# Kernel tuning notes

Measured on AMD Instinct MI355X. Metric: run time of the kernel, lower is better.

The kernel has to match this reference:

```python
import jax, jax.numpy as jnp
import numpy as np


def setup_inputs() -> dict:
    key = jax.random.key(0)
    k1, k2, k3 = jax.random.split(key, 3)
    vol_shape = (4, 1, 128, 192, 192)   # [B, C, D, H, W]
    dsc_shape = (4, 1, 8, 12, 12)       # PatchGAN-style discriminator logits
    return {
        "dsc_fake": jax.random.normal(k1, dsc_shape, dtype=jnp.float32),
        "predicts": jax.random.normal(k2, vol_shape, dtype=jnp.float32),
        "y_data": jax.random.normal(k3, vol_shape, dtype=jnp.float32),
        "zeros": jnp.zeros(dsc_shape, dtype=jnp.float32),
    }


def reference(dsc_fake, predicts, y_data, zeros):
    # BCE with logits (stable form), target = zeros
    bce = jnp.mean(
        jnp.maximum(dsc_fake, 0.0) - dsc_fake * zeros
        + jnp.log1p(jnp.exp(-jnp.abs(dsc_fake)))
    )
    # L1 loss between target volume and prediction
    g_loss_l1 = jnp.mean(jnp.abs(y_data - predicts))
    # Finite-difference gradient MSE along D, H, W (axes 2,3,4).
    # Original detaches to numpy, so this term carries no gradient.
    yd = jax.lax.stop_gradient(y_data)
    pr = jax.lax.stop_gradient(predicts)
    g_loss_gd = jnp.float32(0.0)
    for ax in (2, 3, 4):
        gy = jnp.abs(jnp.gradient(yd, axis=ax))   # central diff interior, one-sided edges
        gp = jnp.abs(jnp.gradient(pr, axis=ax))
        g_loss_gd = g_loss_gd + jnp.mean((gy - gp) ** 2)
    return bce + 100.0 * g_loss_l1 + 100.0 * g_loss_gd
```

## Files before the change

kernel.cpp:

```cpp
#include <hip/hip_runtime.h>
#include <math.h>

namespace {
constexpr int BATCH = 4;
constexpr int DDIM  = 128;
constexpr int HDIM  = 192;
constexpr int WDIM  = 192;
constexpr long long NTOT = (long long)BATCH * DDIM * HDIM * WDIM;
constexpr int GW   = WDIM / 4;
constexpr int HS4  = GW;
constexpr int DS4  = GW * HDIM;
constexpr int NDSC = 4 * 1 * 8 * 12 * 12;
constexpr int BLOCK = 256;
constexpr int DC    = 8;
constexpr int NCH   = DDIM / DC;
constexpr int NCOL  = BATCH * HDIM * GW;
constexpr int NTHREADS = NCOL * NCH;
constexpr int GRID  = NTHREADS / BLOCK;
}

__device__ __forceinline__ float4 ld4(const float* __restrict__ p, long long g) {
    return *(const float4*)(p + 4LL * g);
}

__global__ __launch_bounds__(BLOCK) void vol_kernel(const float* __restrict__ p,
                                                    const float* __restrict__ y,
                                                    float* __restrict__ part) {
    const int t   = blockIdx.x * BLOCK + threadIdx.x;
    const int gw  = t % GW;
    int rest      = t / GW;
    const int h   = rest % HDIM; rest /= HDIM;
    const int b   = rest % BATCH;
    const int d0  = (rest / BATCH) * DC;

    const int   hmo = (h > 0)        ? HS4 : 0;
    const int   hpo = (h < HDIM - 1) ? HS4 : 0;
    const float sh  = (h == 0 || h == HDIM - 1) ? 1.f : 0.5f;
    const int   wlo = (gw > 0)       ? -1 : 0;
    const int   wro = (gw < GW - 1)  ? 4 : 3;
    const float swx = (gw == 0)      ? 1.f : 0.5f;
    const float sww = (gw == GW - 1) ? 1.f : 0.5f;

    long long g = (((long long)b * DDIM + d0) * HDIM + h) * GW + gw;

    const long long gm = g - ((d0 > 0) ? DS4 : 0);
    float4 ym = ld4(y, gm), pm = ld4(p, gm);
    float4 yc = ld4(y, g),  pc = ld4(p, g);
    long long gn = g + DS4;
    float4 yn = ld4(y, gn), pn = ld4(p, gn);
    float4 yhm = ld4(y, g - hmo), yhp = ld4(y, g + hpo);
    float4 phm = ld4(p, g - hmo), php = ld4(p, g + hpo);
    float ywl = y[4LL * g + wlo], ywr = y[4LL * g + wro];
    float pwl = p[4LL * g + wlo], pwr = p[4LL * g + wro];

    float l1 = 0.f, gd = 0.f;

    #pragma unroll
    for (int i = 0; i < DC; ++i) {
        const int d = d0 + i;

        float4 ynn, pnn, yhm2, yhp2, phm2, php2;
        float ywl2, ywr2, pwl2, pwr2;
        long long gnn = gn;
        if (i < DC - 1) {
            gnn = gn + ((d + 2 < DDIM) ? DS4 : 0);
            ynn  = ld4(y, gnn);      pnn  = ld4(p, gnn);
            yhm2 = ld4(y, gn - hmo); yhp2 = ld4(y, gn + hpo);
            phm2 = ld4(p, gn - hmo); php2 = ld4(p, gn + hpo);
            ywl2 = y[4LL * gn + wlo]; ywr2 = y[4LL * gn + wro];
            pwl2 = p[4LL * gn + wlo]; pwr2 = p[4LL * gn + wro];
        }

        const float sd = (d == 0 || d == DDIM - 1) ? 1.f : 0.5f;

        l1 += fabsf(yc.x - pc.x) + fabsf(yc.y - pc.y)
            + fabsf(yc.z - pc.z) + fabsf(yc.w - pc.w);

        float t0, gy, gp;
        gy = (yc.y - ywl) * swx;  gp = (pc.y - pwl) * swx;
        t0 = fabsf(gy) - fabsf(gp); gd += t0 * t0;
        gy = (yc.z - yc.x) * 0.5f; gp = (pc.z - pc.x) * 0.5f;
        t0 = fabsf(gy) - fabsf(gp); gd += t0 * t0;
        gy = (yc.w - yc.y) * 0.5f; gp = (pc.w - pc.y) * 0.5f;
        t0 = fabsf(gy) - fabsf(gp); gd += t0 * t0;
        gy = (ywr - yc.z) * sww;  gp = (pwr - pc.z) * sww;
        t0 = fabsf(gy) - fabsf(gp); gd += t0 * t0;

        t0 = fabsf((yhp.x - yhm.x) * sh) - fabsf((php.x - phm.x) * sh); gd += t0 * t0;
        t0 = fabsf((yhp.y - yhm.y) * sh) - fabsf((php.y - phm.y) * sh); gd += t0 * t0;
        t0 = fabsf((yhp.z - yhm.z) * sh) - fabsf((php.z - phm.z) * sh); gd += t0 * t0;
        t0 = fabsf((yhp.w - yhm.w) * sh) - fabsf((php.w - phm.w) * sh); gd += t0 * t0;

        t0 = fabsf((yn.x - ym.x) * sd) - fabsf((pn.x - pm.x) * sd); gd += t0 * t0;
        t0 = fabsf((yn.y - ym.y) * sd) - fabsf((pn.y - pm.y) * sd); gd += t0 * t0;
        t0 = fabsf((yn.z - ym.z) * sd) - fabsf((pn.z - pm.z) * sd); gd += t0 * t0;
        t0 = fabsf((yn.w - ym.w) * sd) - fabsf((pn.w - pm.w) * sd); gd += t0 * t0;

        if (i < DC - 1) {
            ym = yc; yc = yn; yn = ynn;
            pm = pc; pc = pn; pn = pnn;
            yhm = yhm2; yhp = yhp2; phm = phm2; php = php2;
            ywl = ywl2; ywr = ywr2; pwl = pwl2; pwr = pwr2;
            g = gn; gn = gnn;
        }
    }

    __shared__ float lds1[4], lds2[4];
    #pragma unroll
    for (int off = 32; off > 0; off >>= 1) {
        l1 += __shfl_down(l1, off, 64);
        gd += __shfl_down(gd, off, 64);
    }
    if ((threadIdx.x & 63) == 0) {
        lds1[threadIdx.x >> 6] = l1;
        lds2[threadIdx.x >> 6] = gd;
    }
    __syncthreads();
    if (threadIdx.x == 0) {
        part[2 * blockIdx.x]     = lds1[0] + lds1[1] + lds1[2] + lds1[3];
        part[2 * blockIdx.x + 1] = lds2[0] + lds2[1] + lds2[2] + lds2[3];
    }
}

__global__ __launch_bounds__(BLOCK) void finalize_kernel(const float* __restrict__ dsc,
                                                         const float* __restrict__ part,
                                                         float* __restrict__ out) {
    float l1 = 0.f, gd = 0.f, s = 0.f;
    for (int i = threadIdx.x; i < GRID; i += BLOCK) {
        l1 += part[2 * i];
        gd += part[2 * i + 1];
    }
    for (int i = threadIdx.x; i < NDSC; i += BLOCK) {
        const float x = dsc[i];
        s += fmaxf(x, 0.f) + log1pf(expf(-fabsf(x)));
    }
    __shared__ float a[4], c[4], e[4];
    #pragma unroll
    for (int off = 32; off > 0; off >>= 1) {
        l1 += __shfl_down(l1, off, 64);
        gd += __shfl_down(gd, off, 64);
        s  += __shfl_down(s,  off, 64);
    }
    if ((threadIdx.x & 63) == 0) {
        const int w = threadIdx.x >> 6;
        a[w] = l1; c[w] = gd; e[w] = s;
    }
    __syncthreads();
    if (threadIdx.x == 0) {
        const float bce = (e[0] + e[1] + e[2] + e[3]) / (float)NDSC;
        const float l1m = (a[0] + a[1] + a[2] + a[3]) / (float)NTOT;
        const float gdm = (c[0] + c[1] + c[2] + c[3]) / (float)NTOT;
        out[0] = bce + 100.f * (l1m + gdm);
    }
}

extern "C" void kernel_launch(void* const* d_in, const int* in_sizes, int n_in,
                              void* d_out, int out_size, void* d_ws, size_t ws_size,
                              hipStream_t stream) {
    const float* dsc_fake = (const float*)d_in[0];
    const float* predicts = (const float*)d_in[1];
    const float* y_data   = (const float*)d_in[2];
    float* part = (float*)d_ws;
    float* out  = (float*)d_out;

    vol_kernel<<<GRID, BLOCK, 0, stream>>>(predicts, y_data, part);
    finalize_kernel<<<1, BLOCK, 0, stream>>>(dsc_fake, part, out);
}
```

Measured before the change: 193.4 us.

## Stage HxW slabs in LDS via async global_load_lds with triple-buffered D sweep

The volume kernel now gives each block a 12-row H tile with halo across 16 D planes. Each plane of y and p is staged into LDS with async global-to-LDS loads in a three-deep ring, and H/W neighbours are read from shared memory instead of re-read from global. This cuts the redundant global traffic of the old per-thread stencil, which loaded H neighbours and W edge scalars separately, and overlaps plane prefetch with compute using explicit waitcnt and barriers. The cost is large LDS use per block, a smaller grid of 512 blocks of 192 threads, and fragile hand-written vmcnt accounting.

Result: no change. 190.2 us (-1.6%).

```diff
diff --git a/kernel.cpp b/kernel.cpp
--- a/kernel.cpp
+++ b/kernel.cpp
@@ -7,134 +7,198 @@
 constexpr int HDIM  = 192;
 constexpr int WDIM  = 192;
 constexpr long long NTOT = (long long)BATCH * DDIM * HDIM * WDIM;
-constexpr int GW   = WDIM / 4;
-constexpr int HS4  = GW;
-constexpr int DS4  = GW * HDIM;
-constexpr int NDSC = 4 * 1 * 8 * 12 * 12;
-constexpr int BLOCK = 256;
-constexpr int DC    = 8;
-constexpr int NCH   = DDIM / DC;
-constexpr int NCOL  = BATCH * HDIM * GW;
-constexpr int NTHREADS = NCOL * NCH;
-constexpr int GRID  = NTHREADS / BLOCK;
-}
-
-__device__ __forceinline__ float4 ld4(const float* __restrict__ p, long long g) {
-    return *(const float4*)(p + 4LL * g);
-}
-
-__global__ __launch_bounds__(BLOCK) void vol_kernel(const float* __restrict__ p,
-                                                    const float* __restrict__ y,
-                                                    float* __restrict__ part) {
-    const int t   = blockIdx.x * BLOCK + threadIdx.x;
-    const int gw  = t % GW;
-    int rest      = t / GW;
-    const int h   = rest % HDIM; rest /= HDIM;
-    const int b   = rest % BATCH;
-    const int d0  = (rest / BATCH) * DC;
-
-    const int   hmo = (h > 0)        ? HS4 : 0;
-    const int   hpo = (h < HDIM - 1) ? HS4 : 0;
-    const float sh  = (h == 0 || h == HDIM - 1) ? 1.f : 0.5f;
-    const int   wlo = (gw > 0)       ? -1 : 0;
-    const int   wro = (gw < GW - 1)  ? 4 : 3;
-    const float swx = (gw == 0)      ? 1.f : 0.5f;
-    const float sww = (gw == GW - 1) ? 1.f : 0.5f;
-
-    long long g = (((long long)b * DDIM + d0) * HDIM + h) * GW + gw;
-
-    const long long gm = g - ((d0 > 0) ? DS4 : 0);
-    float4 ym = ld4(y, gm), pm = ld4(p, gm);
-    float4 yc = ld4(y, g),  pc = ld4(p, g);
-    long long gn = g + DS4;
-    float4 yn = ld4(y, gn), pn = ld4(p, gn);
-    float4 yhm = ld4(y, g - hmo), yhp = ld4(y, g + hpo);
-    float4 phm = ld4(p, g - hmo), php = ld4(p, g + hpo);
-    float ywl = y[4LL * g + wlo], ywr = y[4LL * g + wro];
-    float pwl = p[4LL * g + wlo], pwr = p[4LL * g + wro];
+constexpr int NDSC  = 4 * 1 * 8 * 12 * 12;
+
+constexpr int HT     = 12;
+constexpr int DT     = 16;
+constexpr int ROWS   = HT + 2;
+constexpr int SLABF  = ROWS * WDIM;
+constexpr int SLAB2  = 2 * SLABF;
+constexpr int BLOCKV = 192;
+constexpr int GRIDV  = BATCH * (DDIM / DT) * (HDIM / HT);
+constexpr int UPW    = 7;
+constexpr int PLSTR  = HDIM * WDIM;
+constexpr int BLOCKF = 256;
+}
+
+#define GTERM(dy, dp, s2) { float t0_ = fabsf(dy) - fabsf(dp); gd = fmaf(t0_ * t0_, (s2), gd); }
+
+#define STAGE(buf, plane)                                                      \
+    {                                                                          \
+        const int poff_ = (plane) * PLSTR;                                     \
+        _Pragma("unroll")                                                      \
+        for (int k = 0; k < UPW; ++k) {                                        \
+            __builtin_amdgcn_global_load_lds(                                  \
+                (const __attribute__((address_space(1))) void*)(sr[k] + poff_),\
+                (__attribute__((address_space(3))) void*)(                     \
+                    &slab[buf][0] + (wv * UPW + k) * 256),                     \
+                16, 0, 0);                                                     \
+        }                                                                      \
+    }
+
+__global__ __launch_bounds__(BLOCKV) void vol_kernel(const float* __restrict__ p,
+                                                     const float* __restrict__ y,
+                                                     float* __restrict__ part) {
+    __shared__ float slab[3][SLAB2];
+    __shared__ float red[2][3];
+
+    const int tid  = threadIdx.x;
+    const int wv   = tid >> 6;
+    const int lane = tid & 63;
+    const int r    = tid >> 4;
+    const int i16  = tid & 15;
+    const int w0   = i16 * 12;
+
+    const int blk = blockIdx.x;
+    const int ht = blk & 15;
+    const int dc = (blk >> 4) & 7;
+    const int b  = blk >> 7;
+    const int h0 = ht * HT;
+    const int d0 = dc * DT;
+    const int h  = h0 + r;
+
+    const float* sr[UPW];
+    #pragma unroll
+    for (int k = 0; k < UPW; ++k) {
+        const int u   = wv * UPW + k;
+        const int fi  = u * 256 + lane * 4;
+        const int ts  = fi >= SLABF;
+        const int fj  = ts ? fi - SLABF : fi;
+        const int row = fj / WDIM;
+        const int col = fj - row * WDIM;
+        int hrow = h0 - 1 + row;
+        hrow = hrow < 0 ? 0 : (hrow > HDIM - 1 ? HDIM - 1 : hrow);
+        sr[k] = (ts ? p : y) + (b * DDIM * HDIM + hrow) * WDIM + col;
+    }
+
+    float4 ym[2][3], yc[2][3];
+    {
+        const int pmz = d0 ? d0 - 1 : 0;
+        const int om = ((b * DDIM + pmz) * HDIM + h) * WDIM + w0;
+        const int oc = ((b * DDIM + d0 ) * HDIM + h) * WDIM + w0;
+        #pragma unroll
+        for (int g = 0; g < 3; ++g) {
+            ym[0][g] = *(const float4*)(y + om + 4 * g);
+            ym[1][g] = *(const float4*)(p + om + 4 * g);
+            yc[0][g] = *(const float4*)(y + oc + 4 * g);
+            yc[1][g] = *(const float4*)(p + oc + 4 * g);
+        }
+    }
+    STAGE(0, d0);
+    STAGE(1, d0 + 1);
+    STAGE(2, d0 + 2);
 
     float l1 = 0.f, gd = 0.f;
-
-    #pragma unroll
-    for (int i = 0; i < DC; ++i) {
-        const int d = d0 + i;
-
-        float4 ynn, pnn, yhm2, yhp2, phm2, php2;
-        float ywl2, ywr2, pwl2, pwr2;
-        long long gnn = gn;
-        if (i < DC - 1) {
-            gnn = gn + ((d + 2 < DDIM) ? DS4 : 0);
-            ynn  = ld4(y, gnn);      pnn  = ld4(p, gnn);
-            yhm2 = ld4(y, gn - hmo); yhp2 = ld4(y, gn + hpo);
-            phm2 = ld4(p, gn - hmo); php2 = ld4(p, gn + hpo);
-            ywl2 = y[4LL * gn + wlo]; ywr2 = y[4LL * gn + wro];
-            pwl2 = p[4LL * gn + wlo]; pwr2 = p[4LL * gn + wro];
-        }
-
-        const float sd = (d == 0 || d == DDIM - 1) ? 1.f : 0.5f;
-
-        l1 += fabsf(yc.x - pc.x) + fabsf(yc.y - pc.y)
-            + fabsf(yc.z - pc.z) + fabsf(yc.w - pc.w);
-
-        float t0, gy, gp;
-        gy = (yc.y - ywl) * swx;  gp = (pc.y - pwl) * swx;
-        t0 = fabsf(gy) - fabsf(gp); gd += t0 * t0;
-        gy = (yc.z - yc.x) * 0.5f; gp = (pc.z - pc.x) * 0.5f;
-        t0 = fabsf(gy) - fabsf(gp); gd += t0 * t0;
-        gy = (yc.w - yc.y) * 0.5f; gp = (pc.w - pc.y) * 0.5f;
-        t0 = fabsf(gy) - fabsf(gp); gd += t0 * t0;
-        gy = (ywr - yc.z) * sww;  gp = (pwr - pc.z) * sww;
-        t0 = fabsf(gy) - fabsf(gp); gd += t0 * t0;
-
-        t0 = fabsf((yhp.x - yhm.x) * sh) - fabsf((php.x - phm.x) * sh); gd += t0 * t0;
-        t0 = fabsf((yhp.y - yhm.y) * sh) - fabsf((php.y - phm.y) * sh); gd += t0 * t0;
-        t0 = fabsf((yhp.z - yhm.z) * sh) - fabsf((php.z - phm.z) * sh); gd += t0 * t0;
-        t0 = fabsf((yhp.w - yhm.w) * sh) - fabsf((php.w - phm.w) * sh); gd += t0 * t0;
-
-        t0 = fabsf((yn.x - ym.x) * sd) - fabsf((pn.x - pm.x) * sd); gd += t0 * t0;
-        t0 = fabsf((yn.y - ym.y) * sd) - fabsf((pn.y - pm.y) * sd); gd += t0 * t0;
-        t0 = fabsf((yn.z - ym.z) * sd) - fabsf((pn.z - pm.z) * sd); gd += t0 * t0;
-        t0 = fabsf((yn.w - ym.w) * sd) - fabsf((pn.w - pm.w) * sd); gd += t0 * t0;
-
-        if (i < DC - 1) {
-            ym = yc; yc = yn; yn = ynn;
-            pm = pc; pc = pn; pn = pnn;
-            yhm = yhm2; yhp = yhp2; phm = phm2; php = php2;
-            ywl = ywl2; ywr = ywr2; pwl = pwl2; pwr = pwr2;
-            g = gn; gn = gnn;
-        }
-    }
-
-    __shared__ float lds1[4], lds2[4];
+    const float s2h  = (h == 0 || h == HDIM - 1) ? 1.f : 0.25f;
+    const float s2w0 = (i16 == 0)  ? 1.f : 0.25f;
+    const float s2w3 = (i16 == 15) ? 1.f : 0.25f;
+
+    int cur = 0;
+    #pragma unroll 1
+    for (int i = 0; i < DT; ++i) {
+        const int e = d0 + i;
+        if (i == DT - 1) { asm volatile("s_waitcnt vmcnt(0)" ::: "memory"); }
+        else             { asm volatile("s_waitcnt vmcnt(7)" ::: "memory"); }
+        __builtin_amdgcn_sched_barrier(0);
+        __builtin_amdgcn_s_barrier();
+        __builtin_amdgcn_sched_barrier(0);
+
+        const int nxt = (cur == 2) ? 0 : cur + 1;
+        const float* cs = &slab[cur][0];
+        const float* ns = &slab[nxt][0];
+        const float s2d = (e == 0 || e == DDIM - 1) ? 1.f : 0.25f;
+
+        const int rowc = (r + 1) * WDIM;
+        const float wlY = cs[rowc + (i16 ? w0 - 1 : 0)];
+        const float wrY = cs[rowc + (i16 < 15 ? w0 + 12 : WDIM - 1)];
+        const float wlP = cs[SLABF + rowc + (i16 ? w0 - 1 : 0)];
+        const float wrP = cs[SLABF + rowc + (i16 < 15 ? w0 + 12 : WDIM - 1)];
+
+        float4 cn[2][3];
+        #pragma unroll
+        for (int g = 0; g < 3; ++g) {
+            const int off = w0 + 4 * g;
+            const float4 cny = *(const float4*)&ns[rowc + off];
+            const float4 cnp = *(const float4*)&ns[SLABF + rowc + off];
+            const float4 hmy = *(const float4*)&cs[r * WDIM + off];
+            const float4 hpy = *(const float4*)&cs[(r + 2) * WDIM + off];
+            const float4 hmp = *(const float4*)&cs[SLABF + r * WDIM + off];
+            const float4 hpp = *(const float4*)&cs[SLABF + (r + 2) * WDIM + off];
+            cn[0][g] = cny; cn[1][g] = cnp;
+            const float4 ay = yc[0][g], ap = yc[1][g];
+            const float4 my = ym[0][g], mp = ym[1][g];
+
+            l1 += fabsf(ay.x - ap.x) + fabsf(ay.y - ap.y)
+                + fabsf(ay.z - ap.z) + fabsf(ay.w - ap.w);
+            GTERM(hpy.x - hmy.x, hpp.x - hmp.x, s2h);
+            GTERM(hpy.y - hmy.y, hpp.y - hmp.y, s2h);
+            GTERM(hpy.z - hmy.z, hpp.z - hmp.z, s2h);
+            GTERM(hpy.w - hmy.w, hpp.w - hmp.w, s2h);
+            GTERM(cny.x - my.x, cnp.x - mp.x, s2d);
+            GTERM(cny.y - my.y, cnp.y - mp.y, s2d);
+            GTERM(cny.z - my.z, cnp.z - mp.z, s2d);
+            GTERM(cny.w - my.w, cnp.w - mp.w, s2d);
+        }
+        {
+            const float4 a0 = yc[0][0], a1 = yc[0][1], a2 = yc[0][2];
+            const float4 p0 = yc[1][0], p1 = yc[1][1], p2 = yc[1][2];
+            GTERM(a0.y - wlY , p0.y - wlP , s2w0);
+            GTERM(a0.z - a0.x, p0.z - p0.x, 0.25f);
+            GTERM(a0.w - a0.y, p0.w - p0.y, 0.25f);
+            GTERM(a1.x - a0.z, p1.x - p0.z, 0.25f);
+            GTERM(a1.y - a0.w, p1.y - p0.w, 0.25f);
+            GTERM(a1.z - a1.x, p1.z - p1.x, 0.25f);
+            GTERM(a1.w - a1.y, p1.w - p1.y, 0.25f);
+            GTERM(a2.x - a1.z, p2.x - p1.z, 0.25f);
+            GTERM(a2.y - a1.w, p2.y - p1.w, 0.25f);
+            GTERM(a2.z - a2.x, p2.z - p2.x, 0.25f);
+            GTERM(a2.w - a2.y, p2.w - p2.y, 0.25f);
+            GTERM(wrY  - a2.z, wrP  - p2.z, s2w3);
+        }
+        #pragma unroll
+        for (int g = 0; g < 3; ++g) {
+            ym[0][g] = yc[0][g]; ym[1][g] = yc[1][g];
+            yc[0][g] = cn[0][g]; yc[1][g] = cn[1][g];
+        }
+
+        __builtin_amdgcn_sched_barrier(0);
+        asm volatile("s_waitcnt lgkmcnt(0)" ::: "memory");
+        __builtin_amdgcn_sched_barrier(0);
+        __builtin_amdgcn_s_barrier();
+        __builtin_amdgcn_sched_barrier(0);
+        if (i <= DT - 3) {
+            int pl = d0 + i + 3; if (pl > DDIM - 1) pl = DDIM - 1;
+            STAGE(cur, pl);
+        }
+        cur = nxt;
+    }
+
     #pragma unroll
     for (int off = 32; off > 0; off >>= 1) {
         l1 += __shfl_down(l1, off, 64);
         gd += __shfl_down(gd, off, 64);
     }
-    if ((threadIdx.x & 63) == 0) {
-        lds1[threadIdx.x >> 6] = l1;
-        lds2[threadIdx.x >> 6] = gd;
-    }
+    if (lane == 0) { red[0][wv] = l1; red[1][wv] = gd; }
     __syncthreads();
-    if (threadIdx.x == 0) {
-        part[2 * blockIdx.x]     = lds1[0] + lds1[1] + lds1[2] + lds1[3];
-        part[2 * blockIdx.x + 1] = lds2[0] + lds2[1] + lds2[2] + lds2[3];
-    }
-}
-
-__global__ __launch_bounds__(BLOCK) void finalize_kernel(const float* __restrict__ dsc,
-                                                         const float* __restrict__ part,
-                                                         float* __restrict__ out) {
+    if (tid == 0) {
+        part[2 * blk]     = red[0][0] + red[0][1] + red[0][2];
+        part[2 * blk + 1] = red[1][0] + red[1][1] + red[1][2];
+    }
+}
+
+__global__ __launch_bounds__(BLOCKF) void finalize_kernel(const float* __restrict__ dsc,
+                                                          const float* __restrict__ part,
+                                                          float* __restrict__ out) {
     float l1 = 0.f, gd = 0.f, s = 0.f;
-    for (int i = threadIdx.x; i < GRID; i += BLOCK) {
+    for (int i = threadIdx.x; i < GRIDV; i += BLOCKF) {
         l1 += part[2 * i];
         gd += part[2 * i + 1];
     }
-    for (int i = threadIdx.x; i < NDSC; i += BLOCK) {
+    for (int i = threadIdx.x; i < NDSC; i += BLOCKF) {
         const float x = dsc[i];
         s += fmaxf(x, 0.f) + log1pf(expf(-fabsf(x)));
     }
-    __shared__ float a[4], c[4], e[4];
+    __shared__ float a[4], c[4], e2[4];
     #pragma unroll
     for (int off = 32; off > 0; off >>= 1) {
         l1 += __shfl_down(l1, off, 64);
@@ -143,11 +207,11 @@
     }
     if ((threadIdx.x & 63) == 0) {
         const int w = threadIdx.x >> 6;
-        a[w] = l1; c[w] = gd; e[w] = s;
+        a[w] = l1; c[w] = gd; e2[w] = s;
     }
     __syncthreads();
     if (threadIdx.x == 0) {
-        const float bce = (e[0] + e[1] + e[2] + e[3]) / (float)NDSC;
+        const float bce = (e2[0] + e2[1] + e2[2] + e2[3]) / (float)NDSC;
         const float l1m = (a[0] + a[1] + a[2] + a[3]) / (float)NTOT;
         const float gdm = (c[0] + c[1] + c[2] + c[3]) / (float)NTOT;
         out[0] = bce + 100.f * (l1m + gdm);
@@ -163,6 +227,6 @@
     float* part = (float*)d_ws;
     float* out  = (float*)d_out;
 
-    vol_kernel<<<GRID, BLOCK, 0, stream>>>(predicts, y_data, part);
-    finalize_kernel<<<1, BLOCK, 0, stream>>>(dsc_fake, part, out);
-}
+    vol_kernel<<<GRIDV, BLOCKV, 0, stream>>>(predicts, y_data, part);
+    finalize_kernel<<<1, BLOCKF, 0, stream>>>(dsc_fake, part, out);
+}
```
